# Performance work log

Hardware: AMD Instinct MI355X
Metric: run time of the kernel (lower is better)

Reference implementation:

```python
import jax, jax.numpy as jnp
import numpy as np

T, B, IN, H = 512, 256, 256, 256  # time, batch, input dim (hidden_size), GRU state dim (recurrent_input_size)


def setup_inputs() -> dict:
    key = jax.random.key(0)
    ks = jax.random.split(key, 5)
    x = jax.random.normal(ks[0], (T, B, IN), dtype=jnp.float32)
    batch_mask = jax.random.bernoulli(ks[1], 0.5, (T, B))
    rnn_hxs = jax.random.normal(ks[2], (1, B, H), dtype=jnp.float32)
    # PyTorch GRU params, gate order (r, z, n); biases are zero-initialized in the module
    W_ih = jax.random.normal(ks[3], (3 * H, IN), dtype=jnp.float32) * 0.05
    W_hh = jax.random.normal(ks[4], (3 * H, H), dtype=jnp.float32) * 0.05
    b_ih = jnp.zeros((3 * H,), dtype=jnp.float32)
    b_hh = jnp.zeros((3 * H,), dtype=jnp.float32)
    return {"x": x, "rnn_hxs": rnn_hxs, "batch_mask": batch_mask,
            "W_ih": W_ih, "W_hh": W_hh, "b_ih": b_ih, "b_hh": b_hh}


def reference(x, rnn_hxs, batch_mask, W_ih, W_hh, b_ih, b_hh):
    Tn, Bn, In = x.shape
    Hd = rnn_hxs.shape[-1]
    mflat = batch_mask.reshape(-1)                                  # [T*B] row-major (t, b)
    lengths = batch_mask.sum(0)                                     # [B]
    packed = jnp.arange(Tn)[:, None] < lengths[None, :]             # left-aligned mask [T, B]
    pflat = packed.reshape(-1)

    # Faithful emulation of `compact_seq[packed_mask] = x[batch_mask]`:
    # k-th True of packed_mask (row-major) receives k-th True of batch_mask (row-major).
    order = jnp.argsort(jnp.logical_not(mflat), stable=True)        # flat indices of True entries first
    prank = jnp.cumsum(pflat.astype(jnp.int32)) - 1
    src_idx = order[jnp.clip(prank, 0, None)]
    xflat = x.reshape(-1, In)
    compact = jnp.where(pflat[:, None], xflat[src_idx], 0.0).reshape(Tn, Bn, In)

    # GRU over the compacted sequences; hidden frozen past each column's length
    gi_all = jnp.einsum('tbi,gi->tbg', compact, W_ih) + b_ih        # precomputed input projections [T,B,3H]

    def step(h, inp):
        gi, valid = inp                                             # gi: [B,3H], valid: [B]
        gh = h @ W_hh.T + b_hh
        i_r, i_z, i_n = jnp.split(gi, 3, axis=-1)
        h_r, h_z, h_n = jnp.split(gh, 3, axis=-1)
        r = jax.nn.sigmoid(i_r + h_r)
        z = jax.nn.sigmoid(i_z + h_z)
        n = jnp.tanh(i_n + r * h_n)
        h_new = (1.0 - z) * n + z * h
        h_keep = jnp.where(valid[:, None], h_new, h)
        return h_keep, jnp.where(valid[:, None], h_new, 0.0)        # padded steps emit 0 (pad_packed_sequence)

    h_last, seq_out = jax.lax.scan(step, rnn_hxs[0], (gi_all, packed))

    # Faithful emulation of masked_scatter: n-th masked (t,b) position receives
    # the n-th row of scores flattened row-major.
    sflat = seq_out.reshape(-1, Hd)
    rank = jnp.cumsum(mflat.astype(jnp.int32)) - 1
    scores = jnp.where(mflat[:, None], sflat[jnp.clip(rank, 0, None)], 0.0).reshape(Tn, Bn, Hd)
    return scores, h_last[None]
```

## Files before the change

### kernel.cpp

```cpp
#include <hip/hip_runtime.h>
#include <stdint.h>

typedef unsigned short ushortT;
typedef __attribute__((ext_vector_type(8))) short short8;
typedef __attribute__((ext_vector_type(4))) float float4v;
typedef __attribute__((ext_vector_type(4))) int int4v;
typedef __attribute__((ext_vector_type(4))) unsigned short ushort4v;

#define OFF_HDR      0
#define OFF_LEN      8192
#define OFF_CUMM     12288
#define OFF_CUMP     16384
#define OFF_MTI      32768
#define OFF_PARR     557056
#define OFF_WIH      1605632
#define OFF_WHH      1998848
#define OFF_GI       2392064

#define HLAST_OFF    33554432

__device__ __forceinline__ ushortT f2bf(float f) {
  unsigned u = __float_as_uint(f);
  unsigned r = (u + 0x7fffu + ((u >> 16) & 1u)) >> 16;
  return (ushortT)r;
}
__device__ __forceinline__ float bf2f(ushortT h) {
  return __uint_as_float(((unsigned)h) << 16);
}
__device__ __forceinline__ float sigf(float x) { return 1.f / (1.f + __expf(-x)); }
__device__ __forceinline__ float tanhfast(float x) { return 1.f - 2.f / (1.f + __expf(2.f * x)); }

__global__ __launch_bounds__(512) void k_prep(const int* __restrict__ mask, int* __restrict__ wsi) {
  __shared__ int m_s[512], colp[512], len_s[256], sA[512], sB[512];
  __shared__ int sh_mode;
  const int tid = threadIdx.x;
  if (tid == 0) sh_mode = 0;
  __syncthreads();
  int bad = 0;
  for (int i = tid; i < 32768; i += 512) {
    unsigned v = ((const unsigned*)mask)[i];
    if (v > 1u) bad = 1;
  }
  if (bad) atomicOr(&sh_mode, 1);
  __syncthreads();
  const int mode = sh_mode;

  int s = 0;
  if (mode) {
    const unsigned char* mb = (const unsigned char*)mask;
    for (int c = 0; c < 256; c += 4) {
      unsigned v = *(const unsigned*)(mb + tid * 256 + c);
      s += (v & 0xff) + ((v >> 8) & 0xff) + ((v >> 16) & 0xff) + ((v >> 24) & 0xff);
    }
  } else {
    const int4v* mr = (const int4v*)(mask + tid * 256);
    for (int c = 0; c < 64; ++c) { int4v v = mr[c]; s += v[0] + v[1] + v[2] + v[3]; }
  }
  m_s[tid] = s;

  const int b = tid & 255, hh = tid >> 8;
  int cs = 0;
  if (mode) {
    const unsigned char* mb = (const unsigned char*)mask;
    for (int r = hh * 256; r < hh * 256 + 256; ++r) cs += mb[r * 256 + b];
  } else {
    for (int r = hh * 256; r < hh * 256 + 256; ++r) cs += mask[r * 256 + b];
  }
  colp[tid] = cs;
  __syncthreads();
  if (tid < 256) len_s[tid] = colp[tid] + colp[tid + 256];
  __syncthreads();

  int nt = 0;
  for (int i = 0; i < 256; ++i) nt += (len_s[i] > tid) ? 1 : 0;

  sA[tid] = m_s[tid]; sB[tid] = nt;
  for (int off = 1; off < 512; off <<= 1) {
    __syncthreads();
    int am = (tid >= off) ? sA[tid - off] : 0;
    int an = (tid >= off) ? sB[tid - off] : 0;
    __syncthreads();
    sA[tid] += am; sB[tid] += an;
  }
  __syncthreads();
  wsi[OFF_CUMM / 4 + tid] = sA[tid] - m_s[tid];
  wsi[OFF_CUMP / 4 + tid] = sB[tid] - nt;
  if (tid < 256) wsi[OFF_LEN / 4 + tid] = len_s[tid];

  colp[tid] = (tid < 256) ? len_s[tid] : 0;
  for (int off = 256; off >= 1; off >>= 1) {
    __syncthreads();
    int o = (tid < off) ? colp[tid + off] : 0;
    __syncthreads();
    if (tid < off) colp[tid] = max(colp[tid], o);
  }
  __syncthreads();
  if (tid == 0) { wsi[0] = sA[511]; wsi[1] = colp[0]; wsi[2] = mode; }
}

__global__ __launch_bounds__(256) void k_build(const int* __restrict__ mask, int* __restrict__ wsi) {
  const int t = blockIdx.x, b = threadIdx.x;
  const int mode = wsi[2];
  const int lane = b & 63, wv = b >> 6;
  int mflag = mode ? (int)((const unsigned char*)mask)[t * 256 + b] : mask[t * 256 + b];
  mflag = mflag ? 1 : 0;
  const int len = wsi[OFF_LEN / 4 + b];
  const int pflag = (t < len) ? 1 : 0;
  unsigned long long bm = __ballot(mflag), bp = __ballot(pflag);
  __shared__ int wm[4], wp[4];
  if (lane == 0) { wm[wv] = __popcll(bm); wp[wv] = __popcll(bp); }
  __syncthreads();
  int baseM = 0, baseP = 0;
  for (int i = 0; i < wv; ++i) { baseM += wm[i]; baseP += wp[i]; }
  unsigned long long lt = (1ull << lane) - 1ull;
  const int moff = baseM + __popcll(bm & lt);
  const int poff = baseP + __popcll(bp & lt);
  const int j = t * 256 + b;
  if (mflag) wsi[OFF_MTI / 4 + wsi[OFF_CUMM / 4 + t] + moff] = j;
  wsi[OFF_PARR / 4 + j] = pflag ? (wsi[OFF_CUMP / 4 + t] + poff) : -1;
}

__global__ __launch_bounds__(256) void k_wcvt(const float* __restrict__ Wih,
                                              const float* __restrict__ Whh,
                                              int* __restrict__ wsi) {
  const int idx = (blockIdx.x * 256 + threadIdx.x) * 4;
  const float* src;
  ushortT* dst;
  if (idx < 196608) { src = Wih + idx; dst = (ushortT*)((char*)wsi + OFF_WIH) + idx; }
  else { src = Whh + (idx - 196608); dst = (ushortT*)((char*)wsi + OFF_WHH) + (idx - 196608); }
  float4v v = *(const float4v*)src;
  ushort4v o;
  o[0] = f2bf(v[0]); o[1] = f2bf(v[1]); o[2] = f2bf(v[2]); o[3] = f2bf(v[3]);
  *(ushort4v*)dst = o;
}

__global__ __launch_bounds__(256, 2) void k_gemm(const float* __restrict__ x, int* __restrict__ wsi) {
  const int K = wsi[0];
  const int m0 = blockIdx.x * 128;
  if (m0 >= K) return;
  const int n0 = blockIdx.y * 128;
  char* wsc = (char*)wsi;
  const ushortT* Bw = (const ushortT*)(wsc + OFF_WIH);
  ushortT* C = (ushortT*)(wsc + OFF_GI);
  __shared__ ushortT As[128 * 72], Bs[128 * 72];
  __shared__ int mti_s[128];
  const int tid = threadIdx.x, w = tid >> 6, lane = tid & 63;
  const int l15 = lane & 15, quad = lane >> 4;
  if (tid < 128) {
    int m = m0 + tid;
    mti_s[tid] = (m < K) ? wsi[OFF_MTI / 4 + m] : 0;
  }
  float4v acc[4][4];
#pragma unroll
  for (int i = 0; i < 4; ++i)
#pragma unroll
    for (int j = 0; j < 4; ++j) acc[i][j] = (float4v){0.f, 0.f, 0.f, 0.f};

  for (int k0 = 0; k0 < 256; k0 += 64) {
    __syncthreads();
#pragma unroll
    for (int i = 0; i < 8; ++i) {
      int cid = i * 256 + tid;
      int row = cid >> 4, c4 = cid & 15;
      float4v v = *(const float4v*)(x + (size_t)mti_s[row] * 256 + k0 + c4 * 4);
      ushort4v o;
      o[0] = f2bf(v[0]); o[1] = f2bf(v[1]); o[2] = f2bf(v[2]); o[3] = f2bf(v[3]);
      *(ushort4v*)(As + row * 72 + c4 * 4) = o;
    }
#pragma unroll
    for (int i = 0; i < 4; ++i) {
      int cid = i * 256 + tid;
      int row = cid >> 3, c8 = cid & 7;
      int4v vb = *(const int4v*)(Bw + (size_t)(n0 + row) * 256 + k0 + c8 * 8);
      *(int4v*)(Bs + row * 72 + c8 * 8) = vb;
    }
    __syncthreads();
#pragma unroll
    for (int kk = 0; kk < 2; ++kk) {
      short8 af[4], bfr[4];
#pragma unroll
      for (int i = 0; i < 4; ++i)
        af[i] = *(const short8*)(As + ((w >> 1) * 64 + i * 16 + l15) * 72 + kk * 32 + quad * 8);
#pragma unroll
      for (int j = 0; j < 4; ++j)
        bfr[j] = *(const short8*)(Bs + ((w & 1) * 64 + j * 16 + l15) * 72 + kk * 32 + quad * 8);
#pragma unroll
      for (int i = 0; i < 4; ++i)
#pragma unroll
        for (int j = 0; j < 4; ++j)
          acc[i][j] = __builtin_amdgcn_mfma_f32_16x16x32_bf16(af[i], bfr[j], acc[i][j], 0, 0, 0);
    }
  }
#pragma unroll
  for (int i = 0; i < 4; ++i) {
    int m = m0 + (w >> 1) * 64 + i * 16 + quad * 4;
#pragma unroll
    for (int j = 0; j < 4; ++j) {
      int n = n0 + (w & 1) * 64 + j * 16 + l15;
#pragma unroll
      for (int r = 0; r < 4; ++r)
        if (m + r < K) C[(size_t)(m + r) * 768 + n] = f2bf(acc[i][j][r]);
    }
  }
}

__global__ __launch_bounds__(512, 2) void k_rec(const float* __restrict__ bih,
                                                const float* __restrict__ bhh,
                                                const float* __restrict__ h0,
                                                int* __restrict__ wsi,
                                                float* __restrict__ out) {
  const int b0 = blockIdx.x * 16;
  const int tid = threadIdx.x;
  const int w = tid >> 6, lane = tid & 63, l15 = lane & 15, quad = lane >> 4;
  char* wsc = (char*)wsi;
  const ushortT* Whh = (const ushortT*)(wsc + OFF_WHH);
  const ushortT* gib = (const ushortT*)(wsc + OFF_GI);
  const int* parr = wsi + OFF_PARR / 4;
  const int* mti = wsi + OFF_MTI / 4;
  const int K = wsi[0];

  __shared__ float gh_s[16 * 770];
  __shared__ ushortT hbf[16 * 264];
  __shared__ float bih_s[768], bhh_s[768];
  __shared__ int len_s[16];

  for (int i = tid; i < 768; i += 512) { bih_s[i] = bih[i]; bhh_s[i] = bhh[i]; }
  if (tid < 16) len_s[tid] = wsi[OFF_LEN / 4 + b0 + tid];

  short8 wf[6][8];
#pragma unroll
  for (int tt = 0; tt < 6; ++tt) {
    int n = w * 96 + tt * 16 + l15;
#pragma unroll
    for (int kk = 0; kk < 8; ++kk)
      wf[tt][kk] = *(const short8*)(Whh + n * 256 + kk * 32 + quad * 8);
  }

  const int bB = tid >> 5;
  const int bg = b0 + bB;
  const int c0 = (tid & 31) * 8;
  float hreg[8];
  {
    float4v a = *(const float4v*)(h0 + bg * 256 + c0);
    float4v b = *(const float4v*)(h0 + bg * 256 + c0 + 4);
    hreg[0] = a[0]; hreg[1] = a[1]; hreg[2] = a[2]; hreg[3] = a[3];
    hreg[4] = b[0]; hreg[5] = b[1]; hreg[6] = b[2]; hreg[7] = b[3];
    ushort4v p0, p1;
    p0[0] = f2bf(a[0]); p0[1] = f2bf(a[1]); p0[2] = f2bf(a[2]); p0[3] = f2bf(a[3]);
    p1[0] = f2bf(b[0]); p1[1] = f2bf(b[1]); p1[2] = f2bf(b[2]); p1[3] = f2bf(b[3]);
    *(ushort4v*)(hbf + bB * 264 + c0) = p0;
    *(ushort4v*)(hbf + bB * 264 + c0 + 4) = p1;
  }
  __syncthreads();

  int tmax = 0;
#pragma unroll
  for (int i = 0; i < 16; ++i) tmax = max(tmax, len_s[i]);

  int pcur = parr[bg];
  int mcur = mti[bg];
  int4v gi_r, gi_z, gi_n;
  {
    size_t pb = (size_t)max(pcur, 0) * 768;
    gi_r = *(const int4v*)(gib + pb + c0);
    gi_z = *(const int4v*)(gib + pb + 256 + c0);
    gi_n = *(const int4v*)(gib + pb + 512 + c0);
  }

  for (int t = 0; t < tmax; ++t) {
    int pnext = -1, mnext = 0;
    if (t + 1 < 512) {
      pnext = parr[(t + 1) * 256 + bg];
      mnext = mti[(t + 1) * 256 + bg];
    }

    float4v acc[6];
#pragma unroll
    for (int tt = 0; tt < 6; ++tt) acc[tt] = (float4v){0.f, 0.f, 0.f, 0.f};
#pragma unroll
    for (int kk = 0; kk < 8; ++kk) {
      short8 a = *(const short8*)((const char*)hbf + l15 * 528 + kk * 64 + quad * 16);
#pragma unroll
      for (int tt = 0; tt < 6; ++tt)
        acc[tt] = __builtin_amdgcn_mfma_f32_16x16x32_bf16(a, wf[tt][kk], acc[tt], 0, 0, 0);
    }
#pragma unroll
    for (int tt = 0; tt < 6; ++tt) {
      int n = w * 96 + tt * 16 + l15;
#pragma unroll
      for (int r = 0; r < 4; ++r)
        gh_s[(quad * 4 + r) * 770 + n] = acc[tt][r];
    }
    __syncthreads();

    const bool valid = (t < len_s[bB]);
    const int nflat = t * 256 + bg;
    float4v ghr0 = *(const float4v*)(gh_s + bB * 770 + c0);
    float4v ghr1 = *(const float4v*)(gh_s + bB * 770 + c0 + 4);
    float4v ghz0 = *(const float4v*)(gh_s + bB * 770 + 256 + c0);
    float4v ghz1 = *(const float4v*)(gh_s + bB * 770 + 256 + c0 + 4);
    float4v ghn0 = *(const float4v*)(gh_s + bB * 770 + 512 + c0);
    float4v ghn1 = *(const float4v*)(gh_s + bB * 770 + 512 + c0 + 4);
#pragma unroll
    for (int j = 0; j < 8; ++j) {
      float ghr = (j < 4) ? ghr0[j & 3] : ghr1[j & 3];
      float ghz = (j < 4) ? ghz0[j & 3] : ghz1[j & 3];
      float ghn = (j < 4) ? ghn0[j & 3] : ghn1[j & 3];
      float gr = bf2f((ushortT)(((unsigned)gi_r[j >> 1]) >> ((j & 1) * 16)));
      float gz = bf2f((ushortT)(((unsigned)gi_z[j >> 1]) >> ((j & 1) * 16)));
      float gn = bf2f((ushortT)(((unsigned)gi_n[j >> 1]) >> ((j & 1) * 16)));
      float rr = sigf(gr + bih_s[c0 + j] + ghr + bhh_s[c0 + j]);
      float zz = sigf(gz + bih_s[256 + c0 + j] + ghz + bhh_s[256 + c0 + j]);
      float nn = tanhfast(gn + bih_s[512 + c0 + j] + rr * (ghn + bhh_s[512 + c0 + j]));
      float hv = (1.f - zz) * nn + zz * hreg[j];
      hreg[j] = valid ? hv : hreg[j];
    }
    if (valid && nflat < K) {
      float4v o0 = {hreg[0], hreg[1], hreg[2], hreg[3]};
      float4v o1 = {hreg[4], hreg[5], hreg[6], hreg[7]};
      *(float4v*)(out + (size_t)mcur * 256 + c0) = o0;
      *(float4v*)(out + (size_t)mcur * 256 + c0 + 4) = o1;
    }
    {
      ushort4v p0, p1;
      p0[0] = f2bf(hreg[0]); p0[1] = f2bf(hreg[1]); p0[2] = f2bf(hreg[2]); p0[3] = f2bf(hreg[3]);
      p1[0] = f2bf(hreg[4]); p1[1] = f2bf(hreg[5]); p1[2] = f2bf(hreg[6]); p1[3] = f2bf(hreg[7]);
      *(ushort4v*)(hbf + bB * 264 + c0) = p0;
      *(ushort4v*)(hbf + bB * 264 + c0 + 4) = p1;
    }
    {
      size_t pb = (size_t)max(pnext, 0) * 768;
      gi_r = *(const int4v*)(gib + pb + c0);
      gi_z = *(const int4v*)(gib + pb + 256 + c0);
      gi_n = *(const int4v*)(gib + pb + 512 + c0);
    }
    pcur = pnext; mcur = mnext;
    __syncthreads();
  }

  {
    float4v o0 = {hreg[0], hreg[1], hreg[2], hreg[3]};
    float4v o1 = {hreg[4], hreg[5], hreg[6], hreg[7]};
    *(float4v*)(out + HLAST_OFF + (size_t)bg * 256 + c0) = o0;
    *(float4v*)(out + HLAST_OFF + (size_t)bg * 256 + c0 + 4) = o1;
  }
}

extern "C" void kernel_launch(void* const* d_in, const int* in_sizes, int n_in,
                              void* d_out, int out_size, void* d_ws, size_t ws_size,
                              hipStream_t stream) {
  const float* x = (const float*)d_in[0];
  const float* h0 = (const float*)d_in[1];
  const int* mask = (const int*)d_in[2];
  const float* Wih = (const float*)d_in[3];
  const float* Whh = (const float*)d_in[4];
  const float* bih = (const float*)d_in[5];
  const float* bhh = (const float*)d_in[6];
  float* out = (float*)d_out;
  int* wsi = (int*)d_ws;

  hipMemsetAsync(d_out, 0, (size_t)out_size * 4, stream);

  k_prep<<<1, 512, 0, stream>>>(mask, wsi);
  k_build<<<512, 256, 0, stream>>>(mask, wsi);
  k_wcvt<<<384, 256, 0, stream>>>(Wih, Whh, wsi);
  k_gemm<<<dim3(1024, 6), 256, 0, stream>>>(x, wsi);
  k_rec<<<16, 512, 0, stream>>>(bih, bhh, h0, wsi, out);
}
```

Measured before the change: 1.581 ms.

## Use LDS-only barriers, register biases, split column mapping in GRU recurrence

```diff
diff --git a/kernel.cpp b/kernel.cpp
--- a/kernel.cpp
+++ b/kernel.cpp
@@ -5,6 +5,7 @@
 typedef __attribute__((ext_vector_type(8))) short short8;
 typedef __attribute__((ext_vector_type(4))) float float4v;
 typedef __attribute__((ext_vector_type(4))) int int4v;
+typedef __attribute__((ext_vector_type(2))) int int2v;
 typedef __attribute__((ext_vector_type(4))) unsigned short ushort4v;
 
 #define OFF_HDR      0
@@ -29,6 +30,10 @@
 }
 __device__ __forceinline__ float sigf(float x) { return 1.f / (1.f + __expf(-x)); }
 __device__ __forceinline__ float tanhfast(float x) { return 1.f - 2.f / (1.f + __expf(2.f * x)); }
+
+__device__ __forceinline__ void bar_lds() {
+  asm volatile("s_waitcnt lgkmcnt(0)\n\ts_barrier" ::: "memory");
+}
 
 __global__ __launch_bounds__(512) void k_prep(const int* __restrict__ mask, int* __restrict__ wsi) {
   __shared__ int m_s[512], colp[512], len_s[256], sA[512], sB[512];
@@ -219,12 +224,10 @@
   const int* mti = wsi + OFF_MTI / 4;
   const int K = wsi[0];
 
-  __shared__ float gh_s[16 * 770];
+  __shared__ float gh_s[16 * 772];
   __shared__ ushortT hbf[16 * 264];
-  __shared__ float bih_s[768], bhh_s[768];
   __shared__ int len_s[16];
 
-  for (int i = tid; i < 768; i += 512) { bih_s[i] = bih[i]; bhh_s[i] = bhh[i]; }
   if (tid < 16) len_s[tid] = wsi[OFF_LEN / 4 + b0 + tid];
 
   short8 wf[6][8];
@@ -238,18 +241,27 @@
 
   const int bB = tid >> 5;
   const int bg = b0 + bB;
-  const int c0 = (tid & 31) * 8;
-  float hreg[8];
+  const int cA = (tid & 31) * 4;
+  const int cB = cA + 128;
+
+  float4v brA = *(const float4v*)(bih + cA)        + *(const float4v*)(bhh + cA);
+  float4v brB = *(const float4v*)(bih + cB)        + *(const float4v*)(bhh + cB);
+  float4v bzA = *(const float4v*)(bih + 256 + cA)  + *(const float4v*)(bhh + 256 + cA);
+  float4v bzB = *(const float4v*)(bih + 256 + cB)  + *(const float4v*)(bhh + 256 + cB);
+  float4v binA = *(const float4v*)(bih + 512 + cA);
+  float4v binB = *(const float4v*)(bih + 512 + cB);
+  float4v bhnA = *(const float4v*)(bhh + 512 + cA);
+  float4v bhnB = *(const float4v*)(bhh + 512 + cB);
+  const int lenB = ((const int*)((char*)wsi + OFF_LEN))[bg];
+
+  float4v hA = *(const float4v*)(h0 + bg * 256 + cA);
+  float4v hB = *(const float4v*)(h0 + bg * 256 + cB);
   {
-    float4v a = *(const float4v*)(h0 + bg * 256 + c0);
-    float4v b = *(const float4v*)(h0 + bg * 256 + c0 + 4);
-    hreg[0] = a[0]; hreg[1] = a[1]; hreg[2] = a[2]; hreg[3] = a[3];
-    hreg[4] = b[0]; hreg[5] = b[1]; hreg[6] = b[2]; hreg[7] = b[3];
     ushort4v p0, p1;
-    p0[0] = f2bf(a[0]); p0[1] = f2bf(a[1]); p0[2] = f2bf(a[2]); p0[3] = f2bf(a[3]);
-    p1[0] = f2bf(b[0]); p1[1] = f2bf(b[1]); p1[2] = f2bf(b[2]); p1[3] = f2bf(b[3]);
-    *(ushort4v*)(hbf + bB * 264 + c0) = p0;
-    *(ushort4v*)(hbf + bB * 264 + c0 + 4) = p1;
+#pragma unroll
+    for (int j = 0; j < 4; ++j) { p0[j] = f2bf(hA[j]); p1[j] = f2bf(hB[j]); }
+    *(ushort4v*)(hbf + bB * 264 + cA) = p0;
+    *(ushort4v*)(hbf + bB * 264 + cB) = p1;
   }
   __syncthreads();
 
@@ -259,12 +271,12 @@
 
   int pcur = parr[bg];
   int mcur = mti[bg];
-  int4v gi_r, gi_z, gi_n;
+  int2v giA_r, giA_z, giA_n, giB_r, giB_z, giB_n;
   {
-    size_t pb = (size_t)max(pcur, 0) * 768;
-    gi_r = *(const int4v*)(gib + pb + c0);
-    gi_z = *(const int4v*)(gib + pb + 256 + c0);
-    gi_n = *(const int4v*)(gib + pb + 512 + c0);
+    const ushortT* gp = gib + (size_t)max(pcur, 0) * 768;
+    giA_r = *(const int2v*)(gp + cA);       giB_r = *(const int2v*)(gp + cB);
+    giA_z = *(const int2v*)(gp + 256 + cA); giB_z = *(const int2v*)(gp + 256 + cB);
+    giA_n = *(const int2v*)(gp + 512 + cA); giB_n = *(const int2v*)(gp + 512 + cB);
   }
 
   for (int t = 0; t < tmax; ++t) {
@@ -289,61 +301,61 @@
       int n = w * 96 + tt * 16 + l15;
 #pragma unroll
       for (int r = 0; r < 4; ++r)
-        gh_s[(quad * 4 + r) * 770 + n] = acc[tt][r];
-    }
-    __syncthreads();
-
-    const bool valid = (t < len_s[bB]);
+        gh_s[(quad * 4 + r) * 772 + n] = acc[tt][r];
+    }
+    bar_lds();
+
+    const bool valid = (t < lenB);
     const int nflat = t * 256 + bg;
-    float4v ghr0 = *(const float4v*)(gh_s + bB * 770 + c0);
-    float4v ghr1 = *(const float4v*)(gh_s + bB * 770 + c0 + 4);
-    float4v ghz0 = *(const float4v*)(gh_s + bB * 770 + 256 + c0);
-    float4v ghz1 = *(const float4v*)(gh_s + bB * 770 + 256 + c0 + 4);
-    float4v ghn0 = *(const float4v*)(gh_s + bB * 770 + 512 + c0);
-    float4v ghn1 = *(const float4v*)(gh_s + bB * 770 + 512 + c0 + 4);
-#pragma unroll
-    for (int j = 0; j < 8; ++j) {
-      float ghr = (j < 4) ? ghr0[j & 3] : ghr1[j & 3];
-      float ghz = (j < 4) ? ghz0[j & 3] : ghz1[j & 3];
-      float ghn = (j < 4) ? ghn0[j & 3] : ghn1[j & 3];
-      float gr = bf2f((ushortT)(((unsigned)gi_r[j >> 1]) >> ((j & 1) * 16)));
-      float gz = bf2f((ushortT)(((unsigned)gi_z[j >> 1]) >> ((j & 1) * 16)));
-      float gn = bf2f((ushortT)(((unsigned)gi_n[j >> 1]) >> ((j & 1) * 16)));
-      float rr = sigf(gr + bih_s[c0 + j] + ghr + bhh_s[c0 + j]);
-      float zz = sigf(gz + bih_s[256 + c0 + j] + ghz + bhh_s[256 + c0 + j]);
-      float nn = tanhfast(gn + bih_s[512 + c0 + j] + rr * (ghn + bhh_s[512 + c0 + j]));
-      float hv = (1.f - zz) * nn + zz * hreg[j];
-      hreg[j] = valid ? hv : hreg[j];
+    float4v ghrA = *(const float4v*)(gh_s + bB * 772 + cA);
+    float4v ghrB = *(const float4v*)(gh_s + bB * 772 + cB);
+    float4v ghzA = *(const float4v*)(gh_s + bB * 772 + 256 + cA);
+    float4v ghzB = *(const float4v*)(gh_s + bB * 772 + 256 + cB);
+    float4v ghnA = *(const float4v*)(gh_s + bB * 772 + 512 + cA);
+    float4v ghnB = *(const float4v*)(gh_s + bB * 772 + 512 + cB);
+#pragma unroll
+    for (int j = 0; j < 4; ++j) {
+      float grA = bf2f((ushortT)(((unsigned)giA_r[j >> 1]) >> ((j & 1) * 16)));
+      float gzA = bf2f((ushortT)(((unsigned)giA_z[j >> 1]) >> ((j & 1) * 16)));
+      float gnA = bf2f((ushortT)(((unsigned)giA_n[j >> 1]) >> ((j & 1) * 16)));
+      float rr = sigf(grA + ghrA[j] + brA[j]);
+      float zz = sigf(gzA + ghzA[j] + bzA[j]);
+      float nn = tanhfast(gnA + binA[j] + rr * (ghnA[j] + bhnA[j]));
+      float hv = nn + zz * (hA[j] - nn);
+      hA[j] = valid ? hv : hA[j];
+
+      float grB = bf2f((ushortT)(((unsigned)giB_r[j >> 1]) >> ((j & 1) * 16)));
+      float gzB = bf2f((ushortT)(((unsigned)giB_z[j >> 1]) >> ((j & 1) * 16)));
+      float gnB = bf2f((ushortT)(((unsigned)giB_n[j >> 1]) >> ((j & 1) * 16)));
+      float rr2 = sigf(grB + ghrB[j] + brB[j]);
+      float zz2 = sigf(gzB + ghzB[j] + bzB[j]);
+      float nn2 = tanhfast(gnB + binB[j] + rr2 * (ghnB[j] + bhnB[j]));
+      float hv2 = nn2 + zz2 * (hB[j] - nn2);
+      hB[j] = valid ? hv2 : hB[j];
     }
     if (valid && nflat < K) {
-      float4v o0 = {hreg[0], hreg[1], hreg[2], hreg[3]};
-      float4v o1 = {hreg[4], hreg[5], hreg[6], hreg[7]};
-      *(float4v*)(out + (size_t)mcur * 256 + c0) = o0;
-      *(float4v*)(out + (size_t)mcur * 256 + c0 + 4) = o1;
+      *(float4v*)(out + (size_t)mcur * 256 + cA) = hA;
+      *(float4v*)(out + (size_t)mcur * 256 + cB) = hB;
     }
     {
       ushort4v p0, p1;
-      p0[0] = f2bf(hreg[0]); p0[1] = f2bf(hreg[1]); p0[2] = f2bf(hreg[2]); p0[3] = f2bf(hreg[3]);
-      p1[0] = f2bf(hreg[4]); p1[1] = f2bf(hreg[5]); p1[2] = f2bf(hreg[6]); p1[3] = f2bf(hreg[7]);
-      *(ushort4v*)(hbf + bB * 264 + c0) = p0;
-      *(ushort4v*)(hbf + bB * 264 + c0 + 4) = p1;
+#pragma unroll
+      for (int j = 0; j < 4; ++j) { p0[j] = f2bf(hA[j]); p1[j] = f2bf(hB[j]); }
+      *(ushort4v*)(hbf + bB * 264 + cA) = p0;
+      *(ushort4v*)(hbf + bB * 264 + cB) = p1;
     }
     {
-      size_t pb = (size_t)max(pnext, 0) * 768;
-      gi_r = *(const int4v*)(gib + pb + c0);
-      gi_z = *(const int4v*)(gib + pb + 256 + c0);
-      gi_n = *(const int4v*)(gib + pb + 512 + c0);
+      const ushortT* gp = gib + (size_t)max(pnext, 0) * 768;
+      giA_r = *(const int2v*)(gp + cA);       giB_r = *(const int2v*)(gp + cB);
+      giA_z = *(const int2v*)(gp + 256 + cA); giB_z = *(const int2v*)(gp + 256 + cB);
+      giA_n = *(const int2v*)(gp + 512 + cA); giB_n = *(const int2v*)(gp + 512 + cB);
     }
     pcur = pnext; mcur = mnext;
-    __syncthreads();
-  }
-
-  {
-    float4v o0 = {hreg[0], hreg[1], hreg[2], hreg[3]};
-    float4v o1 = {hreg[4], hreg[5], hreg[6], hreg[7]};
-    *(float4v*)(out + HLAST_OFF + (size_t)bg * 256 + c0) = o0;
-    *(float4v*)(out + HLAST_OFF + (size_t)bg * 256 + c0 + 4) = o1;
-  }
+    bar_lds();
+  }
+
+  *(float4v*)(out + HLAST_OFF + (size_t)bg * 256 + cA) = hA;
+  *(float4v*)(out + HLAST_OFF + (size_t)bg * 256 + cB) = hB;
 }
 
 extern "C" void kernel_launch(void* const* d_in, const int* in_sizes, int n_in,
```

Measured after the change: 1.833 ms. 1.16x slower.
